# Kernel tuning notes

Hardware: AMD Instinct MI355X
Metric: run time of the kernel (lower is better)

Reference implementation:

```python
import jax, jax.numpy as jnp
import numpy as np

IN_CH, D, K = 256, 128, 512

def setup_inputs() -> dict:
    key = jax.random.key(0)
    k1, k2, k3, k4 = jax.random.split(key, 4)
    x = jax.random.normal(k1, (16, IN_CH, 64, 64), dtype=jnp.float32)
    W = jax.random.normal(k2, (D, IN_CH), dtype=jnp.float32) * (1.0 / np.sqrt(IN_CH))
    b = jax.random.normal(k3, (D,), dtype=jnp.float32) * 0.01
    prototypes = jax.random.normal(k4, (K, D), dtype=jnp.float32) * 0.02
    gamma = jnp.asarray(1.0, dtype=jnp.float32)
    return {"x": x, "W": W, "b": b, "prototypes": prototypes, "gamma": gamma}

def reference(x, W, b, prototypes, gamma):
    n, c, h, w = x.shape
    # 1x1 conv projection: [n,c,h,w] -> [n,h,w,d]
    q = jnp.einsum('nchw,dc->nhwd', x, W) + b
    q_flat = q.reshape(n * h * w, -1)                      # [T, d]
    q_norm2 = jnp.sum(q_flat * q_flat, axis=1, keepdims=True)   # [T, 1]
    p_norm2 = jnp.sum(prototypes * prototypes, axis=1)[None, :] # [1, K]
    dist2 = q_norm2 + p_norm2 - 2.0 * (q_flat @ prototypes.T)   # [T, K]
    weights = jax.nn.softmax(-jnp.abs(gamma) * dist2, axis=1)
    return weights.reshape(n, h, w, -1).transpose(0, 3, 1, 2)   # [n, K, h, w]
```

## Files before the change

### kernel.cpp

```cpp
#include <hip/hip_runtime.h>

#define HW 4096
#define NCH 256
#define DIM 128
#define NPROTO 512

typedef __attribute__((ext_vector_type(4))) float f32x4;
typedef __attribute__((ext_vector_type(8))) short s16x8;

__device__ __forceinline__ unsigned short f2bf(float f) {
  union { float f; unsigned u; } v; v.f = f;
  unsigned r = v.u + 0x7fffu + ((v.u >> 16) & 1u);
  return (unsigned short)(r >> 16);
}

__global__ __launch_bounds__(256) void prep_kernel(const float* __restrict__ P,
                                                   const float* __restrict__ Wm,
                                                   unsigned short* __restrict__ Pr,
                                                   unsigned short* __restrict__ Wbf,
                                                   float* __restrict__ pn2) {
  const int tid = threadIdx.x;
  const int b = blockIdx.x;
  if (b < 8) {
    const int n  = b * 64 + (tid >> 2);
    const int qt = tid & 3;
    const float* row = P + n * DIM + qt * 32;
    unsigned short* dst = Pr + ((size_t)qt * NPROTO + n) * 32;
    float ssq = 0.f;
#pragma unroll
    for (int u = 0; u < 8; ++u) {
      f32x4 v = *(const f32x4*)(row + 4 * u);
      ssq += v.x * v.x + v.y * v.y + v.z * v.z + v.w * v.w;
      dst[4 * u + 0] = f2bf(v.x);
      dst[4 * u + 1] = f2bf(v.y);
      dst[4 * u + 2] = f2bf(v.z);
      dst[4 * u + 3] = f2bf(v.w);
    }
    ssq += __shfl_xor(ssq, 1);
    ssq += __shfl_xor(ssq, 2);
    if (qt == 0) pn2[n] = ssq;
  } else {
    const int idx = ((b - 8) * 256 + tid) * 16;
#pragma unroll
    for (int u = 0; u < 4; ++u) {
      f32x4 v = *(const f32x4*)(Wm + idx + 4 * u);
      unsigned short* d = Wbf + idx + 4 * u;
      d[0] = f2bf(v.x); d[1] = f2bf(v.y); d[2] = f2bf(v.z); d[3] = f2bf(v.w);
    }
  }
}

__global__ __launch_bounds__(512, 4) void fused_kernel(
    const float* __restrict__ x, const unsigned short* __restrict__ Wbf,
    const float* __restrict__ bias, const unsigned short* __restrict__ Pr,
    const float* __restrict__ pn2, const float* __restrict__ gptr,
    float* __restrict__ out) {
  __shared__ __align__(16) char smem[18688];
  unsigned short* q_s = (unsigned short*)smem;
  char* x_b = smem + 8192;
  float* red  = (float*)(smem + 17408);
  float* rmx  = (float*)(smem + 18432);
  float* rinv = (float*)(smem + 18560);

  const int tid  = threadIdx.x;
  const int p0   = blockIdx.x * 32;
  const int nimg = p0 >> 12;
  const int hw0  = p0 & 4095;
  const int wave = tid >> 6, lane = tid & 63;
  const int l15 = lane & 15, l4 = lane >> 4;

  const int dloc = 16 * wave + l15;
  s16x8 wf[8];
  {
    const unsigned short* wrow = Wbf + (size_t)dloc * NCH + 8 * l4;
#pragma unroll
    for (int k = 0; k < 8; ++k) wf[k] = *(const s16x8*)(wrow + 32 * k);
  }

  const float* xb = x + (size_t)nimg * NCH * HW + hw0;
  const int f  = tid & 7;
  const int cp = tid >> 3;
  f32x4 xv[4][2];
  if (tid < 256) {
#pragma unroll
    for (int it = 0; it < 4; ++it) {
      xv[it][0] = *(const f32x4*)(xb + (size_t)(64 * it + 2 * cp + 0) * HW + 4 * f);
      xv[it][1] = *(const f32x4*)(xb + (size_t)(64 * it + 2 * cp + 1) * HW + 4 * f);
    }
  }
  const float bv = bias[dloc];

  f32x4 acc1[2];
#pragma unroll
  for (int i = 0; i < 2; ++i)
#pragma unroll
    for (int r = 0; r < 4; ++r) acc1[i][r] = 0.f;

#pragma unroll
  for (int it = 0; it < 4; ++it) {
    char* xbuf = x_b + (it & 1) * 4608;
    if (tid < 256) {
#pragma unroll
      for (int s = 0; s < 4; ++s) {
        const int row = 4 * f + s;
        unsigned pk = (unsigned)f2bf(xv[it][0][s]) | ((unsigned)f2bf(xv[it][1][s]) << 16);
        *(unsigned*)(xbuf + row * 144 + ((4 * cp) ^ (((row >> 2) & 7) << 4))) = pk;
      }
    }
    asm volatile("s_waitcnt lgkmcnt(0)" ::: "memory");
    __builtin_amdgcn_s_barrier();
#pragma unroll
    for (int kc = 0; kc < 64; kc += 32) {
      const int ub = (kc >> 3) + l4;
      s16x8 a[2];
#pragma unroll
      for (int i = 0; i < 2; ++i) {
        const int row = 16 * i + l15;
        a[i] = *(const s16x8*)(xbuf + row * 144 + 16 * (ub ^ ((row >> 2) & 7)));
      }
#pragma unroll
      for (int i = 0; i < 2; ++i)
        acc1[i] = __builtin_amdgcn_mfma_f32_16x16x32_bf16(a[i], wf[2 * it + (kc >> 5)],
                                                          acc1[i], 0, 0, 0);
    }
  }

  {
    const int u = dloc >> 3, d7 = dloc & 7;
#pragma unroll
    for (int i = 0; i < 2; ++i) {
      const int pxb = 16 * i + 4 * l4;
#pragma unroll
      for (int r = 0; r < 4; ++r) {
        const int px = pxb + r;
        q_s[px * 128 + ((u ^ (px & 7)) << 3) + d7] = f2bf(acc1[i][r] + bv);
      }
    }
  }

  f32x4 acc[2][4];
#pragma unroll
  for (int i = 0; i < 2; ++i)
#pragma unroll
    for (int j = 0; j < 4; ++j)
#pragma unroll
      for (int r = 0; r < 4; ++r) acc[i][j][r] = 0.f;

  s16x8 bqA[4], bqB[4];
#pragma unroll
  for (int j = 0; j < 4; ++j)
    bqA[j] = *(const s16x8*)(Pr + (size_t)(0 * NPROTO + 64 * wave + 16 * j + l15) * 32 + 8 * l4);
#pragma unroll
  for (int j = 0; j < 4; ++j)
    bqB[j] = *(const s16x8*)(Pr + (size_t)(1 * NPROTO + 64 * wave + 16 * j + l15) * 32 + 8 * l4);
  asm volatile("s_waitcnt lgkmcnt(0)" ::: "memory");
  __builtin_amdgcn_s_barrier();

#define DO_CHUNK(CH, BQ)                                                        \
  {                                                                             \
    s16x8 afr[2];                                                               \
    _Pragma("unroll") for (int i = 0; i < 2; ++i) {                             \
      const int px = 16 * i + l15;                                              \
      afr[i] = *(const s16x8*)&q_s[px * 128 + (((4 * (CH) + l4) ^ (px & 7)) << 3)]; \
    }                                                                           \
    _Pragma("unroll") for (int j = 0; j < 4; ++j)                               \
      _Pragma("unroll") for (int i = 0; i < 2; ++i)                             \
        acc[i][j] = __builtin_amdgcn_mfma_f32_16x16x32_bf16(afr[i], BQ[j], acc[i][j], 0, 0, 0); \
  }

  DO_CHUNK(0, bqA);
#pragma unroll
  for (int j = 0; j < 4; ++j)
    bqA[j] = *(const s16x8*)(Pr + (size_t)(2 * NPROTO + 64 * wave + 16 * j + l15) * 32 + 8 * l4);
  DO_CHUNK(1, bqB);
#pragma unroll
  for (int j = 0; j < 4; ++j)
    bqB[j] = *(const s16x8*)(Pr + (size_t)(3 * NPROTO + 64 * wave + 16 * j + l15) * 32 + 8 * l4);
  DO_CHUNK(2, bqA);
  DO_CHUNK(3, bqB);
#undef DO_CHUNK

  const float g2  = fabsf(gptr[0]) * 1.44269504088896340736f;
  const float tg2 = 2.f * g2;
  float cj[4];
#pragma unroll
  for (int j = 0; j < 4; ++j) cj[j] = g2 * pn2[64 * wave + 16 * j + l15];

#pragma unroll
  for (int i = 0; i < 2; ++i)
#pragma unroll
    for (int r = 0; r < 4; ++r) {
      float m = -1e30f;
#pragma unroll
      for (int j = 0; j < 4; ++j) {
        float lv = fmaf(acc[i][j][r], tg2, -cj[j]);
        acc[i][j][r] = lv;
        m = fmaxf(m, lv);
      }
#pragma unroll
      for (int s = 1; s < 16; s <<= 1) m = fmaxf(m, __shfl_xor(m, s));
      if (l15 == 0) red[wave * 32 + 16 * i + 4 * l4 + r] = m;
    }
  __syncthreads();
  if (tid < 32) {
    float M = red[tid];
#pragma unroll
    for (int w = 1; w < 8; ++w) M = fmaxf(M, red[w * 32 + tid]);
    rmx[tid] = M;
  }
  __syncthreads();

#pragma unroll
  for (int i = 0; i < 2; ++i) {
    const f32x4 Mi = *(const f32x4*)&rmx[16 * i + 4 * l4];
#pragma unroll
    for (int r = 0; r < 4; ++r) {
      float s = 0.f;
#pragma unroll
      for (int j = 0; j < 4; ++j) {
        float e = exp2f(acc[i][j][r] - Mi[r]);
        acc[i][j][r] = e;
        s += e;
      }
#pragma unroll
      for (int t = 1; t < 16; t <<= 1) s += __shfl_xor(s, t);
      if (l15 == 0) red[wave * 32 + 16 * i + 4 * l4 + r] = s;
    }
  }
  __syncthreads();
  if (tid < 32) {
    float S = 0.f;
#pragma unroll
    for (int w = 0; w < 8; ++w) S += red[w * 32 + tid];
    rinv[tid] = 1.f / S;
  }
  __syncthreads();

  float* ob = out + (size_t)nimg * NPROTO * HW + hw0;
#pragma unroll
  for (int i = 0; i < 2; ++i) {
    const f32x4 iv = *(const f32x4*)&rinv[16 * i + 4 * l4];
    const int px = 16 * i + 4 * l4;
#pragma unroll
    for (int j = 0; j < 4; ++j) {
      const int k = 64 * wave + 16 * j + l15;
      f32x4 o = acc[i][j] * iv;
      *(f32x4*)(ob + (size_t)k * HW + px) = o;
    }
  }
}

extern "C" void kernel_launch(void* const* d_in, const int* in_sizes, int n_in,
                              void* d_out, int out_size, void* d_ws, size_t ws_size,
                              hipStream_t stream) {
  const float* x     = (const float*)d_in[0];
  const float* Wm    = (const float*)d_in[1];
  const float* bias  = (const float*)d_in[2];
  const float* prot  = (const float*)d_in[3];
  const float* gamma = (const float*)d_in[4];
  float* out = (float*)d_out;

  unsigned short* Pr_w  = (unsigned short*)d_ws;
  float*          pn2_w = (float*)((char*)d_ws + 131072);
  unsigned short* W_ws  = (unsigned short*)((char*)d_ws + 131072 + 2048);

  prep_kernel<<<16, 256, 0, stream>>>(prot, Wm, Pr_w, W_ws, pn2_w);
  fused_kernel<<<2048, 512, 0, stream>>>(x, W_ws, bias, Pr_w, pn2_w, gamma, out);
}
```

Measured before the change: 220.2 us.

## Process four pixel tiles per block with rolling x-prefetch pipeline

```diff
diff --git a/kernel.cpp b/kernel.cpp
--- a/kernel.cpp
+++ b/kernel.cpp
@@ -63,9 +63,10 @@
   float* rinv = (float*)(smem + 18560);
 
   const int tid  = threadIdx.x;
-  const int p0   = blockIdx.x * 32;
-  const int nimg = p0 >> 12;
-  const int hw0  = p0 & 4095;
+  const int bid  = blockIdx.x;
+  const int pB   = bid * 128;
+  const int nimg = pB >> 12;
+  const int hw0  = pB & 4095;
   const int wave = tid >> 6, lane = tid & 63;
   const int l15 = lane & 15, l4 = lane >> 4;
 
@@ -76,176 +77,190 @@
 #pragma unroll
     for (int k = 0; k < 8; ++k) wf[k] = *(const s16x8*)(wrow + 32 * k);
   }
-
-  const float* xb = x + (size_t)nimg * NCH * HW + hw0;
+  const float* xbB = x + (size_t)nimg * NCH * HW + hw0;
+  float* obB = out + (size_t)nimg * NPROTO * HW + hw0;
   const int f  = tid & 7;
   const int cp = tid >> 3;
-  f32x4 xv[4][2];
+
+  f32x4 xv[2][2];
   if (tid < 256) {
 #pragma unroll
-    for (int it = 0; it < 4; ++it) {
-      xv[it][0] = *(const f32x4*)(xb + (size_t)(64 * it + 2 * cp + 0) * HW + 4 * f);
-      xv[it][1] = *(const f32x4*)(xb + (size_t)(64 * it + 2 * cp + 1) * HW + 4 * f);
+    for (int g = 0; g < 2; ++g) {
+      xv[g][0] = *(const f32x4*)(xbB + (size_t)(64 * g + 2 * cp + 0) * HW + 4 * f);
+      xv[g][1] = *(const f32x4*)(xbB + (size_t)(64 * g + 2 * cp + 1) * HW + 4 * f);
     }
   }
   const float bv = bias[dloc];
-
-  f32x4 acc1[2];
-#pragma unroll
-  for (int i = 0; i < 2; ++i)
-#pragma unroll
-    for (int r = 0; r < 4; ++r) acc1[i][r] = 0.f;
-
-#pragma unroll
-  for (int it = 0; it < 4; ++it) {
-    char* xbuf = x_b + (it & 1) * 4608;
-    if (tid < 256) {
-#pragma unroll
-      for (int s = 0; s < 4; ++s) {
-        const int row = 4 * f + s;
-        unsigned pk = (unsigned)f2bf(xv[it][0][s]) | ((unsigned)f2bf(xv[it][1][s]) << 16);
-        *(unsigned*)(xbuf + row * 144 + ((4 * cp) ^ (((row >> 2) & 7) << 4))) = pk;
-      }
-    }
-    asm volatile("s_waitcnt lgkmcnt(0)" ::: "memory");
-    __builtin_amdgcn_s_barrier();
-#pragma unroll
-    for (int kc = 0; kc < 64; kc += 32) {
-      const int ub = (kc >> 3) + l4;
-      s16x8 a[2];
-#pragma unroll
-      for (int i = 0; i < 2; ++i) {
-        const int row = 16 * i + l15;
-        a[i] = *(const s16x8*)(xbuf + row * 144 + 16 * (ub ^ ((row >> 2) & 7)));
-      }
-#pragma unroll
-      for (int i = 0; i < 2; ++i)
-        acc1[i] = __builtin_amdgcn_mfma_f32_16x16x32_bf16(a[i], wf[2 * it + (kc >> 5)],
-                                                          acc1[i], 0, 0, 0);
-    }
-  }
-
-  {
-    const int u = dloc >> 3, d7 = dloc & 7;
-#pragma unroll
-    for (int i = 0; i < 2; ++i) {
-      const int pxb = 16 * i + 4 * l4;
-#pragma unroll
-      for (int r = 0; r < 4; ++r) {
-        const int px = pxb + r;
-        q_s[px * 128 + ((u ^ (px & 7)) << 3) + d7] = f2bf(acc1[i][r] + bv);
-      }
-    }
-  }
-
-  f32x4 acc[2][4];
-#pragma unroll
-  for (int i = 0; i < 2; ++i)
-#pragma unroll
-    for (int j = 0; j < 4; ++j)
-#pragma unroll
-      for (int r = 0; r < 4; ++r) acc[i][j][r] = 0.f;
-
-  s16x8 bqA[4], bqB[4];
-#pragma unroll
-  for (int j = 0; j < 4; ++j)
-    bqA[j] = *(const s16x8*)(Pr + (size_t)(0 * NPROTO + 64 * wave + 16 * j + l15) * 32 + 8 * l4);
-#pragma unroll
-  for (int j = 0; j < 4; ++j)
-    bqB[j] = *(const s16x8*)(Pr + (size_t)(1 * NPROTO + 64 * wave + 16 * j + l15) * 32 + 8 * l4);
-  asm volatile("s_waitcnt lgkmcnt(0)" ::: "memory");
-  __builtin_amdgcn_s_barrier();
-
-#define DO_CHUNK(CH, BQ)                                                        \
-  {                                                                             \
-    s16x8 afr[2];                                                               \
-    _Pragma("unroll") for (int i = 0; i < 2; ++i) {                             \
-      const int px = 16 * i + l15;                                              \
-      afr[i] = *(const s16x8*)&q_s[px * 128 + (((4 * (CH) + l4) ^ (px & 7)) << 3)]; \
-    }                                                                           \
-    _Pragma("unroll") for (int j = 0; j < 4; ++j)                               \
-      _Pragma("unroll") for (int i = 0; i < 2; ++i)                             \
-        acc[i][j] = __builtin_amdgcn_mfma_f32_16x16x32_bf16(afr[i], BQ[j], acc[i][j], 0, 0, 0); \
-  }
-
-  DO_CHUNK(0, bqA);
-#pragma unroll
-  for (int j = 0; j < 4; ++j)
-    bqA[j] = *(const s16x8*)(Pr + (size_t)(2 * NPROTO + 64 * wave + 16 * j + l15) * 32 + 8 * l4);
-  DO_CHUNK(1, bqB);
-#pragma unroll
-  for (int j = 0; j < 4; ++j)
-    bqB[j] = *(const s16x8*)(Pr + (size_t)(3 * NPROTO + 64 * wave + 16 * j + l15) * 32 + 8 * l4);
-  DO_CHUNK(2, bqA);
-  DO_CHUNK(3, bqB);
-#undef DO_CHUNK
-
   const float g2  = fabsf(gptr[0]) * 1.44269504088896340736f;
   const float tg2 = 2.f * g2;
   float cj[4];
 #pragma unroll
   for (int j = 0; j < 4; ++j) cj[j] = g2 * pn2[64 * wave + 16 * j + l15];
-
-#pragma unroll
-  for (int i = 0; i < 2; ++i)
-#pragma unroll
-    for (int r = 0; r < 4; ++r) {
-      float m = -1e30f;
+  __builtin_amdgcn_sched_barrier(0);
+
+#pragma unroll
+  for (int t = 0; t < 4; ++t) {
+    f32x4 acc1[2];
+#pragma unroll
+    for (int i = 0; i < 2; ++i)
+#pragma unroll
+      for (int r = 0; r < 4; ++r) acc1[i][r] = 0.f;
+
+#pragma unroll
+    for (int it = 0; it < 4; ++it) {
+      const int g = 4 * t + it;
+      char* xbuf = x_b + (g & 1) * 4608;
+      if (tid < 256) {
+#pragma unroll
+        for (int s = 0; s < 4; ++s) {
+          const int row = 4 * f + s;
+          unsigned pk = (unsigned)f2bf(xv[g & 1][0][s]) |
+                        ((unsigned)f2bf(xv[g & 1][1][s]) << 16);
+          *(unsigned*)(xbuf + row * 144 + ((4 * cp) ^ (((row >> 2) & 7) << 4))) = pk;
+        }
+        if (g + 2 < 16) {
+          const int tt = (g + 2) >> 2, cc = ((g + 2) & 3) * 64;
+          xv[g & 1][0] = *(const f32x4*)(xbB + (size_t)(cc + 2 * cp + 0) * HW + 32 * tt + 4 * f);
+          xv[g & 1][1] = *(const f32x4*)(xbB + (size_t)(cc + 2 * cp + 1) * HW + 32 * tt + 4 * f);
+        }
+      }
+      __builtin_amdgcn_sched_barrier(0);
+      asm volatile("s_waitcnt lgkmcnt(0)" ::: "memory");
+      __builtin_amdgcn_s_barrier();
+#pragma unroll
+      for (int kc = 0; kc < 64; kc += 32) {
+        const int ub = (kc >> 3) + l4;
+        s16x8 a[2];
+#pragma unroll
+        for (int i = 0; i < 2; ++i) {
+          const int row = 16 * i + l15;
+          a[i] = *(const s16x8*)(xbuf + row * 144 + 16 * (ub ^ ((row >> 2) & 7)));
+        }
+#pragma unroll
+        for (int i = 0; i < 2; ++i)
+          acc1[i] = __builtin_amdgcn_mfma_f32_16x16x32_bf16(a[i], wf[2 * it + (kc >> 5)],
+                                                            acc1[i], 0, 0, 0);
+      }
+    }
+
+    {
+      const int u = dloc >> 3, d7 = dloc & 7;
+#pragma unroll
+      for (int i = 0; i < 2; ++i) {
+        const int pxb = 16 * i + 4 * l4;
+#pragma unroll
+        for (int r = 0; r < 4; ++r) {
+          const int px = pxb + r;
+          q_s[px * 128 + ((u ^ (px & 7)) << 3) + d7] = f2bf(acc1[i][r] + bv);
+        }
+      }
+    }
+
+    f32x4 acc[2][4];
+#pragma unroll
+    for (int i = 0; i < 2; ++i)
+#pragma unroll
+      for (int j = 0; j < 4; ++j)
+#pragma unroll
+        for (int r = 0; r < 4; ++r) acc[i][j][r] = 0.f;
+
+    s16x8 bqA[4], bqB[4];
+#pragma unroll
+    for (int j = 0; j < 4; ++j)
+      bqA[j] = *(const s16x8*)(Pr + (size_t)(0 * NPROTO + 64 * wave + 16 * j + l15) * 32 + 8 * l4);
+#pragma unroll
+    for (int j = 0; j < 4; ++j)
+      bqB[j] = *(const s16x8*)(Pr + (size_t)(1 * NPROTO + 64 * wave + 16 * j + l15) * 32 + 8 * l4);
+    __builtin_amdgcn_sched_barrier(0);
+    asm volatile("s_waitcnt lgkmcnt(0)" ::: "memory");
+    __builtin_amdgcn_s_barrier();
+
+#define DO_CHUNK(CH, BQ)                                                        \
+    {                                                                           \
+      s16x8 afr[2];                                                             \
+      _Pragma("unroll") for (int i = 0; i < 2; ++i) {                           \
+        const int px = 16 * i + l15;                                            \
+        afr[i] = *(const s16x8*)&q_s[px * 128 + (((4 * (CH) + l4) ^ (px & 7)) << 3)]; \
+      }                                                                         \
+      _Pragma("unroll") for (int j = 0; j < 4; ++j)                             \
+        _Pragma("unroll") for (int i = 0; i < 2; ++i)                           \
+          acc[i][j] = __builtin_amdgcn_mfma_f32_16x16x32_bf16(afr[i], BQ[j], acc[i][j], 0, 0, 0); \
+    }
+
+    DO_CHUNK(0, bqA);
+#pragma unroll
+    for (int j = 0; j < 4; ++j)
+      bqA[j] = *(const s16x8*)(Pr + (size_t)(2 * NPROTO + 64 * wave + 16 * j + l15) * 32 + 8 * l4);
+    __builtin_amdgcn_sched_barrier(0);
+    DO_CHUNK(1, bqB);
+#pragma unroll
+    for (int j = 0; j < 4; ++j)
+      bqB[j] = *(const s16x8*)(Pr + (size_t)(3 * NPROTO + 64 * wave + 16 * j + l15) * 32 + 8 * l4);
+    __builtin_amdgcn_sched_barrier(0);
+    DO_CHUNK(2, bqA);
+    DO_CHUNK(3, bqB);
+#undef DO_CHUNK
+
+#pragma unroll
+    for (int i = 0; i < 2; ++i)
+#pragma unroll
+      for (int r = 0; r < 4; ++r) {
+        float m = -1e30f;
+#pragma unroll
+        for (int j = 0; j < 4; ++j) {
+          float lv = fmaf(acc[i][j][r], tg2, -cj[j]);
+          acc[i][j][r] = lv;
+          m = fmaxf(m, lv);
+        }
+#pragma unroll
+        for (int s = 1; s < 16; s <<= 1) m = fmaxf(m, __shfl_xor(m, s));
+        if (l15 == 0) red[wave * 32 + 16 * i + 4 * l4 + r] = m;
+      }
+    __syncthreads();
+    if (tid < 32) {
+      float M = red[tid];
+#pragma unroll
+      for (int w = 1; w < 8; ++w) M = fmaxf(M, red[w * 32 + tid]);
+      rmx[tid] = M;
+    }
+    __syncthreads();
+
+#pragma unroll
+    for (int i = 0; i < 2; ++i) {
+      const f32x4 Mi = *(const f32x4*)&rmx[16 * i + 4 * l4];
+#pragma unroll
+      for (int r = 0; r < 4; ++r) {
+        float s = 0.f;
+#pragma unroll
+        for (int j = 0; j < 4; ++j) {
+          float e = exp2f(acc[i][j][r] - Mi[r]);
+          acc[i][j][r] = e;
+          s += e;
+        }
+#pragma unroll
+        for (int tt = 1; tt < 16; tt <<= 1) s += __shfl_xor(s, tt);
+        if (l15 == 0) red[wave * 32 + 16 * i + 4 * l4 + r] = s;
+      }
+    }
+    __syncthreads();
+    if (tid < 32) {
+      float S = 0.f;
+#pragma unroll
+      for (int w = 0; w < 8; ++w) S += red[w * 32 + tid];
+      rinv[tid] = 1.f / S;
+    }
+    __syncthreads();
+
+#pragma unroll
+    for (int i = 0; i < 2; ++i) {
+      const f32x4 iv = *(const f32x4*)&rinv[16 * i + 4 * l4];
+      const int px = 16 * i + 4 * l4 + 32 * t;
 #pragma unroll
       for (int j = 0; j < 4; ++j) {
-        float lv = fmaf(acc[i][j][r], tg2, -cj[j]);
-        acc[i][j][r] = lv;
-        m = fmaxf(m, lv);
-      }
-#pragma unroll
-      for (int s = 1; s < 16; s <<= 1) m = fmaxf(m, __shfl_xor(m, s));
-      if (l15 == 0) red[wave * 32 + 16 * i + 4 * l4 + r] = m;
-    }
-  __syncthreads();
-  if (tid < 32) {
-    float M = red[tid];
-#pragma unroll
-    for (int w = 1; w < 8; ++w) M = fmaxf(M, red[w * 32 + tid]);
-    rmx[tid] = M;
-  }
-  __syncthreads();
-
-#pragma unroll
-  for (int i = 0; i < 2; ++i) {
-    const f32x4 Mi = *(const f32x4*)&rmx[16 * i + 4 * l4];
-#pragma unroll
-    for (int r = 0; r < 4; ++r) {
-      float s = 0.f;
-#pragma unroll
-      for (int j = 0; j < 4; ++j) {
-        float e = exp2f(acc[i][j][r] - Mi[r]);
-        acc[i][j][r] = e;
-        s += e;
-      }
-#pragma unroll
-      for (int t = 1; t < 16; t <<= 1) s += __shfl_xor(s, t);
-      if (l15 == 0) red[wave * 32 + 16 * i + 4 * l4 + r] = s;
-    }
-  }
-  __syncthreads();
-  if (tid < 32) {
-    float S = 0.f;
-#pragma unroll
-    for (int w = 0; w < 8; ++w) S += red[w * 32 + tid];
-    rinv[tid] = 1.f / S;
-  }
-  __syncthreads();
-
-  float* ob = out + (size_t)nimg * NPROTO * HW + hw0;
-#pragma unroll
-  for (int i = 0; i < 2; ++i) {
-    const f32x4 iv = *(const f32x4*)&rinv[16 * i + 4 * l4];
-    const int px = 16 * i + 4 * l4;
-#pragma unroll
-    for (int j = 0; j < 4; ++j) {
-      const int k = 64 * wave + 16 * j + l15;
-      f32x4 o = acc[i][j] * iv;
-      *(f32x4*)(ob + (size_t)k * HW + px) = o;
+        const int k = 64 * wave + 16 * j + l15;
+        f32x4 o = acc[i][j] * iv;
+        *(f32x4*)(obB + (size_t)k * HW + px) = o;
+      }
     }
   }
 }
@@ -265,5 +280,5 @@
   unsigned short* W_ws  = (unsigned short*)((char*)d_ws + 131072 + 2048);
 
   prep_kernel<<<16, 256, 0, stream>>>(prot, Wm, Pr_w, W_ws, pn2_w);
-  fused_kernel<<<2048, 512, 0, stream>>>(x, W_ws, bias, Pr_w, pn2_w, gamma, out);
-}
+  fused_kernel<<<512, 512, 0, stream>>>(x, W_ws, bias, Pr_w, pn2_w, gamma, out);
+}
```

Measured after the change: 346.3 us. 1.57x slower.
